# Performance work log

Measured on AMD Instinct MI355X. Metric: run time of the kernel, lower is better.

The kernel has to match this reference:

```python
import jax, jax.numpy as jnp
import numpy as np

B, H, S, D = 4, 16, 2048, 64


def setup_inputs() -> dict:
    key = jax.random.key(0)
    kq, kk, kv = jax.random.split(key, 3)
    q = jax.random.normal(kq, (B, H, S, D), dtype=jnp.float32)
    k = jax.random.normal(kk, (B, H, S, D), dtype=jnp.float32)
    v = jax.random.normal(kv, (B, H, S, D), dtype=jnp.float32)
    # causal mask, broadcastable over batch/heads (True = keep)
    mask = jnp.tril(jnp.ones((S, S), dtype=bool))[None, None, :, :]
    return {"q": q, "k": k, "v": v, "mask": mask}


def reference(q, k, v, mask):
    d_k = q.shape[-1]
    # [..., q, k] scores with full materialization, as in the original
    scores = jnp.einsum("bhqd,bhkd->bhqk", q, k) / jnp.sqrt(jnp.float32(d_k))
    scores = jnp.where(mask, scores, jnp.float32(-jnp.inf))
    attn = jax.nn.softmax(scores, axis=-1)  # stable: single max-subtract, matches manual softmax
    out = jnp.einsum("bhqk,bhkd->bhqd", attn, v)
    return out
```

## Files before the change

kernel.cpp:

```cpp
#include <hip/hip_runtime.h>
#include <hip/hip_bf16.h>
#include <stdint.h>

#define S_LEN 2048
#define D_DIM 64
#define BH    64
#define NQT   16
#define LOG2E 1.44269504088896f
#define THR   8.0f
#define TEN_ELEMS (BH * S_LEN * D_DIM)

typedef __attribute__((ext_vector_type(8)))  short bf16x8;
typedef __attribute__((ext_vector_type(4)))  short s16x4;
typedef __attribute__((ext_vector_type(4)))  float f32x4;
typedef __attribute__((ext_vector_type(16))) float f32x16;
typedef __attribute__((ext_vector_type(4)))  uint32_t u32x4;

__device__ __forceinline__ short f2bf(float f) {
    uint32_t u = __builtin_bit_cast(uint32_t, f);
    u += 0x7FFFu + ((u >> 16) & 1u);
    return (short)(u >> 16);
}

__device__ __forceinline__ uint32_t pkbf(float lo, float hi) {
    __hip_bfloat162 h = __float22bfloat162_rn(make_float2(lo, hi));
    uint32_t r;
    __builtin_memcpy(&r, &h, 4);
    return r;
}

__device__ __forceinline__ float xhalf_max(float v) {
    return fmaxf(v, __shfl_xor(v, 32));
}
__device__ __forceinline__ float xhalf_sum(float v) {
    return v + __shfl_xor(v, 32);
}

__device__ __forceinline__ int swz(int row, int col) {
    return (row * 64 + col) ^ ((row & 7) << 3);
}

#if __has_builtin(__builtin_amdgcn_exp2f)
#define EXP2(x) __builtin_amdgcn_exp2f(x)
#else
#define EXP2(x) exp2f(x)
#endif

typedef __attribute__((address_space(1))) const uint32_t glb_u32;
typedef __attribute__((address_space(3))) uint32_t lds_u32;
__device__ __forceinline__ void llds16(const short* g, short* l) {
    __builtin_amdgcn_global_load_lds((glb_u32*)g, (lds_u32*)l, 16, 0, 0);
}

__global__ __launch_bounds__(256)
void cvt_qk_kernel(const float* __restrict__ Q, const float* __restrict__ K,
                   short* __restrict__ Qb, short* __restrict__ Kimg)
{
    const size_t gid = (size_t)blockIdx.x * 256 + threadIdx.x;
    const size_t off = gid * 8;
    const float sc = 0.125f * LOG2E;
    f32x4 a0 = *(const f32x4*)(Q + off), a1 = *(const f32x4*)(Q + off + 4);
    f32x4 b0 = *(const f32x4*)(K + off), b1 = *(const f32x4*)(K + off + 4);
    bf16x8 qa, kb;
    #pragma unroll
    for (int j = 0; j < 4; ++j) {
        qa[j] = f2bf(a0[j] * sc); qa[4 + j] = f2bf(a1[j] * sc);
        kb[j] = f2bf(b0[j]);      kb[4 + j] = f2bf(b1[j]);
    }
    *(bf16x8*)(Qb + off) = qa;
    const size_t s  = off >> 6;
    const int    d0 = (int)(off & 63);
    const int    row = (int)(s & 63);
    *(bf16x8*)(Kimg + (s >> 6) * 4096 + swz(row, d0)) = kb;
}

__global__ __launch_bounds__(256)
void vt_kernel(const float* __restrict__ V, short* __restrict__ Vimg)
{
    const int kt = blockIdx.x;
    const int bh = blockIdx.y;
    const float* Vp = V + (size_t)bh * S_LEN * D_DIM + (size_t)kt * 64 * D_DIM;
    short* Vo = Vimg + ((size_t)bh * 32 + kt) * 4096;
    __shared__ short T[64][72];
    const int tid = threadIdx.x;
    const int row = tid >> 2, q4 = tid & 3;
    #pragma unroll
    for (int j = 0; j < 4; ++j) {
        f32x4 v = *(const f32x4*)(Vp + row * D_DIM + q4 * 16 + j * 4);
        #pragma unroll
        for (int e = 0; e < 4; ++e) T[row][q4 * 16 + j * 4 + e] = f2bf(v[e]);
    }
    __syncthreads();
    const int d = tid >> 2, kq = tid & 3;
    #pragma unroll
    for (int j = 0; j < 4; ++j) {
        s16x4 w;
        #pragma unroll
        for (int e = 0; e < 4; ++e) w[e] = T[kq * 16 + j * 4 + e][d];
        const int jd = (j == 1) ? 2 : ((j == 2) ? 1 : j);
        *(s16x4*)&Vo[swz(d, kq * 16 + jd * 4)] = w;
    }
}

#define STAGE(kb, buf) do { \
    const short* ks_ = Kimg + ((size_t)bh * 32 + (kb)) * 4096; \
    const short* vs_ = Vimg + ((size_t)bh * 32 + (kb)) * 4096; \
    const int wo_ = wid * 1024; \
    llds16(ks_ + wo_ + lane * 8,       &Kl[buf][wo_]); \
    llds16(ks_ + wo_ + 512 + lane * 8, &Kl[buf][wo_ + 512]); \
    llds16(vs_ + wo_ + lane * 8,       &Vl[buf][wo_]); \
    llds16(vs_ + wo_ + 512 + lane * 8, &Vl[buf][wo_ + 512]); \
} while (0)

#define MKFRAG(dst, sv, R0) do { \
    u32x4 t_; \
    t_[0] = pkbf(sv[(R0)+0], sv[(R0)+1]); \
    t_[1] = pkbf(sv[(R0)+2], sv[(R0)+3]); \
    t_[2] = pkbf(sv[(R0)+4], sv[(R0)+5]); \
    t_[3] = pkbf(sv[(R0)+6], sv[(R0)+7]); \
    dst = __builtin_bit_cast(bf16x8, t_); \
} while (0)

#define PVSTEP(pa, koff, acc0, acc1, b) do { \
    bf16x8 vf0_ = *(const bf16x8*)&Vl[b][swz(lq32,      (koff) + hi * 8)]; \
    bf16x8 vf1_ = *(const bf16x8*)&Vl[b][swz(32 + lq32, (koff) + hi * 8)]; \
    acc0 = __builtin_amdgcn_mfma_f32_32x32x16_bf16(pa, vf0_, acc0, 0, 0, 0); \
    acc1 = __builtin_amdgcn_mfma_f32_32x32x16_bf16(pa, vf1_, acc1, 0, 0, 0); \
} while (0)

#define COMPUTE32(qf, acc0, acc1, mm, ll, q0, kv0, b) do { \
    f32x16 s0_ = (f32x16)0.f, s1_ = (f32x16)0.f; \
    __builtin_amdgcn_s_setprio(1); \
    _Pragma("unroll") for (int c = 0; c < 4; ++c) { \
        bf16x8 k0_ = *(const bf16x8*)&Kl[b][swz(lq32,      c * 16 + hi * 8)]; \
        bf16x8 k1_ = *(const bf16x8*)&Kl[b][swz(32 + lq32, c * 16 + hi * 8)]; \
        s0_ = __builtin_amdgcn_mfma_f32_32x32x16_bf16(k0_, qf[c], s0_, 0, 0, 0); \
        s1_ = __builtin_amdgcn_mfma_f32_32x32x16_bf16(k1_, qf[c], s1_, 0, 0, 0); \
    } \
    __builtin_amdgcn_s_setprio(0); \
    if ((kv0) + 63 > (q0)) {    \
        _Pragma("unroll") for (int r = 0; r < 16; ++r) { \
            const int kvr_ = (r & 3) + 8 * (r >> 2) + 4 * hi; \
            if ((kv0) + kvr_      > (q0) + lq32) s0_[r] = -1e30f; \
            if ((kv0) + 32 + kvr_ > (q0) + lq32) s1_[r] = -1e30f; \
        } \
    } \
    float m0_ = fmaxf(s0_[0], s1_[0]), m1_ = fmaxf(s0_[1], s1_[1]); \
    float m2_ = fmaxf(s0_[2], s1_[2]), m3_ = fmaxf(s0_[3], s1_[3]); \
    _Pragma("unroll") for (int r = 4; r < 16; r += 4) { \
        m0_ = fmaxf(m0_, fmaxf(s0_[r],     s1_[r])); \
        m1_ = fmaxf(m1_, fmaxf(s0_[r + 1], s1_[r + 1])); \
        m2_ = fmaxf(m2_, fmaxf(s0_[r + 2], s1_[r + 2])); \
        m3_ = fmaxf(m3_, fmaxf(s0_[r + 3], s1_[r + 3])); \
    } \
    float pmax_ = xhalf_max(fmaxf(fmaxf(m0_, m1_), fmaxf(m2_, m3_))); \
    if (!__all(pmax_ <= (mm) + THR)) {       \
        const float mn_ = fmaxf((mm), pmax_); \
        const float f_  = EXP2((mm) - mn_); \
        (ll) *= f_; \
        _Pragma("unroll") for (int r = 0; r < 16; ++r) { \
            const float fr_ = __shfl(f_, (r & 3) + 8 * (r >> 2) + 4 * hi); \
            acc0[r] *= fr_; acc1[r] *= fr_; \
        } \
        (mm) = mn_; \
    } \
    float t0_ = 0.f, t1_ = 0.f, t2_ = 0.f, t3_ = 0.f; \
    _Pragma("unroll") for (int r = 0; r < 16; r += 4) { \
        s0_[r]     = EXP2(s0_[r]     - (mm)); s1_[r]     = EXP2(s1_[r]     - (mm)); \
        s0_[r + 1] = EXP2(s0_[r + 1] - (mm)); s1_[r + 1] = EXP2(s1_[r + 1] - (mm)); \
        s0_[r + 2] = EXP2(s0_[r + 2] - (mm)); s1_[r + 2] = EXP2(s1_[r + 2] - (mm)); \
        s0_[r + 3] = EXP2(s0_[r + 3] - (mm)); s1_[r + 3] = EXP2(s1_[r + 3] - (mm)); \
        t0_ += s0_[r]     + s1_[r]; \
        t1_ += s0_[r + 1] + s1_[r + 1]; \
        t2_ += s0_[r + 2] + s1_[r + 2]; \
        t3_ += s0_[r + 3] + s1_[r + 3]; \
    } \
    (ll) += (t0_ + t1_) + (t2_ + t3_);       \
    bf16x8 pa0_, pa1_, pa2_, pa3_; \
    MKFRAG(pa0_, s0_, 0); MKFRAG(pa1_, s0_, 8); \
    MKFRAG(pa2_, s1_, 0); MKFRAG(pa3_, s1_, 8); \
    __builtin_amdgcn_s_setprio(1); \
    PVSTEP(pa0_, 0,  acc0, acc1, b); \
    PVSTEP(pa1_, 16, acc0, acc1, b); \
    PVSTEP(pa2_, 32, acc0, acc1, b); \
    PVSTEP(pa3_, 48, acc0, acc1, b); \
    __builtin_amdgcn_s_setprio(0); \
} while (0)

__global__ __launch_bounds__(256, 2)
void attn_fwd_bf16(const short* __restrict__ Qb, const short* __restrict__ Kimg,
                   const short* __restrict__ Vimg, float* __restrict__ Out)
{
    const int bh   = blockIdx.x;
    const int qt   = NQT - 1 - blockIdx.y;
    const int tid  = threadIdx.x;
    const int wid  = tid >> 6;
    const int lane = tid & 63;
    const int lq32 = lane & 31;
    const int hi   = lane >> 5;

    const int nkv = 2 * qt + 2;

    const short* Qp = Qb + (size_t)bh * S_LEN * D_DIM;
    float*       Op = Out + (size_t)bh * S_LEN * D_DIM;

    __shared__ __align__(16) short Kl[2][64 * 64];
    __shared__ __align__(16) short Vl[2][64 * 64];

    const int q0 = qt * 128 + wid * 32;

    bf16x8 qf[4];
    #pragma unroll
    for (int c = 0; c < 4; ++c)
        qf[c] = *(const bf16x8*)(Qp + (size_t)(q0 + lq32) * D_DIM + c * 16 + hi * 8);

    f32x16 acc0 = (f32x16)0.f, acc1 = (f32x16)0.f;
    float m = -1e30f, l = 0.f;

    STAGE(0, 0);
    __syncthreads();

    for (int j = 0; j < nkv; ++j) {
        const int  buf  = j & 1;
        const bool more = (j + 1) < nkv;
        if (more) STAGE(j + 1, buf ^ 1);
        if (j * 64 <= q0 + 31) COMPUTE32(qf, acc0, acc1, m, l, q0, j * 64, buf);
        if (more) __syncthreads();
    }

    l = xhalf_sum(l);
    const float il = 1.f / l;
    #pragma unroll
    for (int r = 0; r < 16; ++r) {
        const int qr   = (r & 3) + 8 * (r >> 2) + 4 * hi;
        const float vl = __shfl(il, qr);
        Op[(size_t)(q0 + qr) * D_DIM + lq32]      = acc0[r] * vl;
        Op[(size_t)(q0 + qr) * D_DIM + 32 + lq32] = acc1[r] * vl;
    }
}

extern "C" void kernel_launch(void* const* d_in, const int* in_sizes, int n_in,
                              void* d_out, int out_size, void* d_ws, size_t ws_size,
                              hipStream_t stream) {
    const float* q = (const float*)d_in[0];
    const float* k = (const float*)d_in[1];
    const float* v = (const float*)d_in[2];
    float* out = (float*)d_out;
    (void)in_sizes; (void)n_in; (void)out_size; (void)ws_size;

    short* Qb   = (short*)d_ws;
    short* Kimg = Qb + TEN_ELEMS;
    short* Vimg = Kimg + TEN_ELEMS;
    cvt_qk_kernel<<<TEN_ELEMS / 8 / 256, 256, 0, stream>>>(q, k, Qb, Kimg);
    vt_kernel<<<dim3(S_LEN / 64, BH), 256, 0, stream>>>(v, Vimg);
    attn_fwd_bf16<<<dim3(BH, NQT), 256, 0, stream>>>(Qb, Kimg, Vimg, out);
}
```

Measured before the change: 89.27 us.

## Fuse Q conversion into attention kernel, merge K/V prep, remap tile schedule

Q is now read as fp32 and converted and scaled to bf16 directly inside the attention kernel, so the separate Q conversion pass and its workspace round-trip go away. K and V image preparation is merged into one prep kernel, which saves a launch. The attention grid becomes 1D, with a permuted mapping of q-tiles per group of 16 blocks meant to balance the causal workload across concurrently running blocks. The cost is that the attention kernel now loads twice as many Q bytes, with conversion arithmetic in its prologue.

```diff
diff --git a/kernel.cpp b/kernel.cpp
--- a/kernel.cpp
+++ b/kernel.cpp
@@ -53,52 +53,53 @@
 }
 
 __global__ __launch_bounds__(256)
-void cvt_qk_kernel(const float* __restrict__ Q, const float* __restrict__ K,
-                   short* __restrict__ Qb, short* __restrict__ Kimg)
-{
-    const size_t gid = (size_t)blockIdx.x * 256 + threadIdx.x;
-    const size_t off = gid * 8;
-    const float sc = 0.125f * LOG2E;
-    f32x4 a0 = *(const f32x4*)(Q + off), a1 = *(const f32x4*)(Q + off + 4);
-    f32x4 b0 = *(const f32x4*)(K + off), b1 = *(const f32x4*)(K + off + 4);
-    bf16x8 qa, kb;
-    #pragma unroll
-    for (int j = 0; j < 4; ++j) {
-        qa[j] = f2bf(a0[j] * sc); qa[4 + j] = f2bf(a1[j] * sc);
-        kb[j] = f2bf(b0[j]);      kb[4 + j] = f2bf(b1[j]);
-    }
-    *(bf16x8*)(Qb + off) = qa;
-    const size_t s  = off >> 6;
-    const int    d0 = (int)(off & 63);
-    const int    row = (int)(s & 63);
-    *(bf16x8*)(Kimg + (s >> 6) * 4096 + swz(row, d0)) = kb;
-}
-
-__global__ __launch_bounds__(256)
-void vt_kernel(const float* __restrict__ V, short* __restrict__ Vimg)
+void prep_kv(const float* __restrict__ K, const float* __restrict__ V,
+             short* __restrict__ Kimg, short* __restrict__ Vimg)
 {
     const int kt = blockIdx.x;
     const int bh = blockIdx.y;
-    const float* Vp = V + (size_t)bh * S_LEN * D_DIM + (size_t)kt * 64 * D_DIM;
-    short* Vo = Vimg + ((size_t)bh * 32 + kt) * 4096;
-    __shared__ short T[64][72];
     const int tid = threadIdx.x;
-    const int row = tid >> 2, q4 = tid & 3;
-    #pragma unroll
-    for (int j = 0; j < 4; ++j) {
-        f32x4 v = *(const f32x4*)(Vp + row * D_DIM + q4 * 16 + j * 4);
-        #pragma unroll
-        for (int e = 0; e < 4; ++e) T[row][q4 * 16 + j * 4 + e] = f2bf(v[e]);
-    }
-    __syncthreads();
-    const int d = tid >> 2, kq = tid & 3;
-    #pragma unroll
-    for (int j = 0; j < 4; ++j) {
-        s16x4 w;
-        #pragma unroll
-        for (int e = 0; e < 4; ++e) w[e] = T[kq * 16 + j * 4 + e][d];
-        const int jd = (j == 1) ? 2 : ((j == 2) ? 1 : j);
-        *(s16x4*)&Vo[swz(d, kq * 16 + jd * 4)] = w;
+
+    {
+        const float* Kp = K + ((size_t)bh * S_LEN + (size_t)kt * 64) * D_DIM;
+        short* Ko = Kimg + ((size_t)bh * 32 + kt) * 4096;
+        const int row = tid >> 2, d0 = (tid & 3) * 16;
+        const float* src = Kp + row * D_DIM + d0;
+        f32x4 a = *(const f32x4*)(src);
+        f32x4 b = *(const f32x4*)(src + 4);
+        f32x4 c = *(const f32x4*)(src + 8);
+        f32x4 d = *(const f32x4*)(src + 12);
+        bf16x8 w0, w1;
+        #pragma unroll
+        for (int j = 0; j < 4; ++j) {
+            w0[j] = f2bf(a[j]); w0[4 + j] = f2bf(b[j]);
+            w1[j] = f2bf(c[j]); w1[4 + j] = f2bf(d[j]);
+        }
+        *(bf16x8*)&Ko[swz(row, d0)]     = w0;
+        *(bf16x8*)&Ko[swz(row, d0 + 8)] = w1;
+    }
+
+    {
+        const float* Vp = V + ((size_t)bh * S_LEN + (size_t)kt * 64) * D_DIM;
+        short* Vo = Vimg + ((size_t)bh * 32 + kt) * 4096;
+        __shared__ short T[64][72];
+        const int row = tid >> 2, q4 = tid & 3;
+        #pragma unroll
+        for (int j = 0; j < 4; ++j) {
+            f32x4 v = *(const f32x4*)(Vp + row * D_DIM + q4 * 16 + j * 4);
+            #pragma unroll
+            for (int e = 0; e < 4; ++e) T[row][q4 * 16 + j * 4 + e] = f2bf(v[e]);
+        }
+        __syncthreads();
+        const int d = tid >> 2, kq = tid & 3;
+        #pragma unroll
+        for (int j = 0; j < 4; ++j) {
+            s16x4 w;
+            #pragma unroll
+            for (int e = 0; e < 4; ++e) w[e] = T[kq * 16 + j * 4 + e][d];
+            const int jd = (j == 1) ? 2 : ((j == 2) ? 1 : j);
+            *(s16x4*)&Vo[swz(d, kq * 16 + jd * 4)] = w;
+        }
     }
 }
 
@@ -188,11 +189,14 @@
 } while (0)
 
 __global__ __launch_bounds__(256, 2)
-void attn_fwd_bf16(const short* __restrict__ Qb, const short* __restrict__ Kimg,
+void attn_fwd_bf16(const float* __restrict__ Q, const short* __restrict__ Kimg,
                    const short* __restrict__ Vimg, float* __restrict__ Out)
 {
-    const int bh   = blockIdx.x;
-    const int qt   = NQT - 1 - blockIdx.y;
+    const int id   = blockIdx.x;
+    const int bh   = id >> 4;
+    const int k4   = id & 3;
+    const int u4   = (id >> 2) & 3;
+    const int qt   = 4 * ((k4 + u4) & 3) + k4;
     const int tid  = threadIdx.x;
     const int wid  = tid >> 6;
     const int lane = tid & 63;
@@ -201,8 +205,7 @@
 
     const int nkv = 2 * qt + 2;
 
-    const short* Qp = Qb + (size_t)bh * S_LEN * D_DIM;
-    float*       Op = Out + (size_t)bh * S_LEN * D_DIM;
+    float* Op = Out + (size_t)bh * S_LEN * D_DIM;
 
     __shared__ __align__(16) short Kl[2][64 * 64];
     __shared__ __align__(16) short Vl[2][64 * 64];
@@ -210,9 +213,20 @@
     const int q0 = qt * 128 + wid * 32;
 
     bf16x8 qf[4];
-    #pragma unroll
-    for (int c = 0; c < 4; ++c)
-        qf[c] = *(const bf16x8*)(Qp + (size_t)(q0 + lq32) * D_DIM + c * 16 + hi * 8);
+    {
+        const float sc = 0.125f * LOG2E;
+        const float* qp = Q + ((size_t)bh * S_LEN + (size_t)(q0 + lq32)) * D_DIM;
+        #pragma unroll
+        for (int c = 0; c < 4; ++c) {
+            f32x4 x0 = *(const f32x4*)(qp + c * 16 + hi * 8);
+            f32x4 x1 = *(const f32x4*)(qp + c * 16 + hi * 8 + 4);
+            #pragma unroll
+            for (int j = 0; j < 4; ++j) {
+                qf[c][j]     = f2bf(x0[j] * sc);
+                qf[c][4 + j] = f2bf(x1[j] * sc);
+            }
+        }
+    }
 
     f32x16 acc0 = (f32x16)0.f, acc1 = (f32x16)0.f;
     float m = -1e30f, l = 0.f;
@@ -248,10 +262,8 @@
     float* out = (float*)d_out;
     (void)in_sizes; (void)n_in; (void)out_size; (void)ws_size;
 
-    short* Qb   = (short*)d_ws;
-    short* Kimg = Qb + TEN_ELEMS;
+    short* Kimg = (short*)d_ws;
     short* Vimg = Kimg + TEN_ELEMS;
-    cvt_qk_kernel<<<TEN_ELEMS / 8 / 256, 256, 0, stream>>>(q, k, Qb, Kimg);
-    vt_kernel<<<dim3(S_LEN / 64, BH), 256, 0, stream>>>(v, Vimg);
-    attn_fwd_bf16<<<dim3(BH, NQT), 256, 0, stream>>>(Qb, Kimg, Vimg, out);
-}
+    prep_kv<<<dim3(S_LEN / 64, BH), 256, 0, stream>>>(k, v, Kimg, Vimg);
+    attn_fwd_bf16<<<dim3(BH * NQT), 256, 0, stream>>>(q, Kimg, Vimg, out);
+}
```

New measurement: 117.4 us. +31.5%, slower.
